# Performance work log

Hardware: AMD Instinct MI355X
Metric: run time of the kernel (lower is better)

The kernel has to match this reference:

```python
import jax, jax.numpy as jnp
import numpy as np

B, S, D, H = 2, 2048, 2048, 16
HD = D // H

def setup_inputs() -> dict:
    key = jax.random.key(0)
    ks = jax.random.split(key, 6)
    x = jax.random.normal(ks[0], (B, S, D), dtype=jnp.float32)
    # causal mask: 1 where attention allowed, 0 where masked
    mask = jnp.tril(jnp.ones((S, S), dtype=jnp.int32))[None, None, :, :]
    scale_w = 0.02
    W_qkv = jax.random.normal(ks[1], (D, 3 * D), dtype=jnp.float32) * scale_w
    b_qkv = jnp.zeros((3 * D,), dtype=jnp.float32)
    W_proj = jax.random.normal(ks[2], (D, D), dtype=jnp.float32) * scale_w
    b_proj = jnp.zeros((D,), dtype=jnp.float32)
    return {"x": x, "W_qkv": W_qkv, "b_qkv": b_qkv, "W_proj": W_proj, "b_proj": b_proj, "mask": mask}

def reference(x, W_qkv, b_qkv, W_proj, b_proj, mask):
    b, s, d = x.shape
    qkv = x @ W_qkv + b_qkv                       # [b,s,3d]
    qkv = qkv.reshape(b, s, 3, H, HD)
    q = jnp.transpose(qkv[:, :, 0], (0, 2, 1, 3))  # [b,h,s,hd]
    k = jnp.transpose(qkv[:, :, 1], (0, 2, 1, 3))
    v = jnp.transpose(qkv[:, :, 2], (0, 2, 1, 3))
    scale = HD ** -0.5
    attn = jnp.einsum('bhqd,bhkd->bhqk', q, k) * scale
    attn = jnp.where(mask == 0, -jnp.inf, attn)
    attn = jax.nn.softmax(attn, axis=-1)
    # dropout is identity in eval mode
    out = jnp.einsum('bhqk,bhkd->bhqd', attn, v)   # [b,h,s,hd]
    out = jnp.transpose(out, (0, 2, 1, 3)).reshape(b, s, d)
    return out @ W_proj + b_proj
```

## Files before the change

### kernel.cpp

```cpp
#include <hip/hip_runtime.h>
#include <hip/hip_bf16.h>
#include <math.h>

#define BATCH 2
#define SEQ   2048
#define DIM   2048
#define NH    16
#define HD    128
#define QKV_N (3 * DIM)
#define TOKENS (BATCH * SEQ)

typedef __attribute__((ext_vector_type(8))) short bf16x8;
typedef __attribute__((ext_vector_type(4))) float f32x4;

typedef __attribute__((address_space(1))) const void* as1cv;
typedef __attribute__((address_space(3))) void* as3v;

__device__ __forceinline__ short f2bf(float x) {
    unsigned u = __float_as_uint(x);
    u += 0x7fffu + ((u >> 16) & 1u);
    return (short)(u >> 16);
}

__device__ __forceinline__ float bf2f(short x) {
    return __uint_as_float(((unsigned)(unsigned short)x) << 16);
}

__device__ __forceinline__ void gload16(const short* g, short* lds) {
    __builtin_amdgcn_global_load_lds((as1cv)g, (as3v)lds, 16, 0, 0);
}

__global__ __launch_bounds__(256)
void f32_to_bf16_kernel(const float* __restrict__ in, short* __restrict__ out) {
    const size_t i = ((size_t)blockIdx.x * 256 + threadIdx.x) * 8;
    const float4 a = *reinterpret_cast<const float4*>(in + i);
    const float4 b = *reinterpret_cast<const float4*>(in + i + 4);
    bf16x8 v;
    v[0] = f2bf(a.x); v[1] = f2bf(a.y); v[2] = f2bf(a.z); v[3] = f2bf(a.w);
    v[4] = f2bf(b.x); v[5] = f2bf(b.y); v[6] = f2bf(b.z); v[7] = f2bf(b.w);
    *reinterpret_cast<bf16x8*>(out + i) = v;
}

__global__ __launch_bounds__(256)
void transpose_f32_to_bf16(const float* __restrict__ W, short* __restrict__ Wt,
                           int K, int N) {
    __shared__ float t[64][65];
    const int tid = threadIdx.x;
    const int n0 = blockIdx.x * 64;
    const int k0 = blockIdx.y * 64;
    const int tc = tid & 63, tr = tid >> 6;
    #pragma unroll
    for (int i = 0; i < 16; ++i)
        t[tr + i * 4][tc] = W[(size_t)(k0 + tr + i * 4) * N + n0 + tc];
    __syncthreads();
    #pragma unroll
    for (int i = 0; i < 16; ++i)
        Wt[(size_t)(n0 + tr + i * 4) * K + k0 + tc] = f2bf(t[tc][tr + i * 4]);
}

template <bool BF16OUT>
__global__ __launch_bounds__(256, 2)
void gemm_mfma_kernel(const short* __restrict__ A, const short* __restrict__ Bt,
                      const float* __restrict__ bias, void* __restrict__ Cv,
                      int M, int N, int K, int nM) {
    __shared__ short A_lds[2][128 * 64];
    __shared__ short B_lds[2][128 * 64];

    const int tid  = threadIdx.x;
    const int lane = tid & 63;
    const int w    = tid >> 6;
    const int lr   = lane & 15;
    const int lhi  = lane >> 4;
    const int wr   = w >> 1;
    const int wc   = w & 1;

    const int nwg  = gridDim.x;
    const int cpx  = nwg >> 3;
    const int orig = blockIdx.x;
    const int wg   = (orig & 7) * cpx + (orig >> 3);
    const int bm   = (wg % nM) * 128;
    const int bn   = (wg / nM) * 128;

    const int srow   = tid >> 3;
    const int schunk = (tid & 7) ^ (srow & 7);
    const short* gA = A  + (size_t)(bm + srow) * K + schunk * 8;
    const short* gB = Bt + (size_t)(bn + srow) * K + schunk * 8;

    const int nt = K >> 6;

    auto STAGE = [&](int t, int buf) {
        const int ko = t * 64;
        short* la = &A_lds[buf][w * 512];
        short* lb = &B_lds[buf][w * 512];
        #pragma unroll
        for (int i = 0; i < 4; ++i)
            gload16(gA + (size_t)(i * 32) * K + ko, la + i * 2048);
        #pragma unroll
        for (int i = 0; i < 4; ++i)
            gload16(gB + (size_t)(i * 32) * K + ko, lb + i * 2048);
    };

    f32x4 acc[4][4] = {};

    STAGE(0, 0);
    STAGE(1, 1);
    asm volatile("s_waitcnt vmcnt(8)" ::: "memory");
    __builtin_amdgcn_s_barrier();

    int cur = 0;
    for (int t = 0; t < nt; ++t, cur ^= 1) {
        bf16x8 af[2][4], bfr[2][4];
        const short* Ab = &A_lds[cur][0];
        const short* Bb = &B_lds[cur][0];
        #pragma unroll
        for (int ks = 0; ks < 2; ++ks) {
            const int cb = ks * 4 + lhi;
            #pragma unroll
            for (int mi = 0; mi < 4; ++mi) {
                const int r = wr * 64 + mi * 16 + lr;
                af[ks][mi] = *reinterpret_cast<const bf16x8*>(
                    &Ab[r * 64 + ((cb ^ (r & 7)) << 3)]);
            }
            #pragma unroll
            for (int ni = 0; ni < 4; ++ni) {
                const int c = wc * 64 + ni * 16 + lr;
                bfr[ks][ni] = *reinterpret_cast<const bf16x8*>(
                    &Bb[c * 64 + ((cb ^ (c & 7)) << 3)]);
            }
        }
        asm volatile("s_waitcnt lgkmcnt(0)" ::: "memory");
        __builtin_amdgcn_sched_barrier(0);
        __builtin_amdgcn_s_barrier();
        __builtin_amdgcn_sched_barrier(0);

        if (t + 2 < nt) STAGE(t + 2, cur);

        __builtin_amdgcn_s_setprio(1);
        #pragma unroll
        for (int ks = 0; ks < 2; ++ks)
            #pragma unroll
            for (int mi = 0; mi < 4; ++mi)
                #pragma unroll
                for (int ni = 0; ni < 4; ++ni)
                    acc[mi][ni] = __builtin_amdgcn_mfma_f32_16x16x32_bf16(
                        af[ks][mi], bfr[ks][ni], acc[mi][ni], 0, 0, 0);
        __builtin_amdgcn_s_setprio(0);
        __builtin_amdgcn_sched_barrier(0);

        if (t + 2 < nt) {
            asm volatile("s_waitcnt vmcnt(8)" ::: "memory");
            __builtin_amdgcn_s_barrier();
        } else if (t + 1 < nt) {
            asm volatile("s_waitcnt vmcnt(0)" ::: "memory");
            __builtin_amdgcn_s_barrier();
        }
    }

    #pragma unroll
    for (int mi = 0; mi < 4; ++mi) {
        #pragma unroll
        for (int j = 0; j < 4; ++j) {
            const int r = bm + wr * 64 + mi * 16 + lhi * 4 + j;
            #pragma unroll
            for (int ni = 0; ni < 4; ++ni) {
                const int c = bn + wc * 64 + ni * 16 + lr;
                const float v = acc[mi][ni][j] + bias[c];
                if (BF16OUT) ((short*)Cv)[(size_t)r * N + c] = f2bf(v);
                else         ((float*)Cv)[(size_t)r * N + c] = v;
            }
        }
    }
}

__device__ __forceinline__ int swz8(int row) {
    return ((row ^ (row >> 2)) & 7) << 3;
}

__global__ __launch_bounds__(256)
void attn_mfma_kernel(const short* __restrict__ qkv, short* __restrict__ out) {
    __shared__ short K_lds[64 * 128];
    __shared__ short V_lds[128 * 64];
    __shared__ short P_lds[4 * 16 * 64];

    const int tid  = threadIdx.x;
    const int lane = tid & 63;
    const int w    = tid >> 6;

    const int z    = blockIdx.x;
    const int qblk = (SEQ / 64 - 1) - (z >> 5);
    const int bh   = z & 31;
    const int h    = bh & 15;
    const int b    = bh >> 4;

    const int q0 = qblk * 64;
    const size_t tokbase = (size_t)b * SEQ * QKV_N;

    const int lr  = lane & 15;
    const int lhi = lane >> 4;
    const float scale = 0.08838834764831845f;

    const int qrow = q0 + w * 16 + lr;
    const short* qrowp = qkv + tokbase + (size_t)qrow * QKV_N + h * HD;
    bf16x8 qfrag[4];
    #pragma unroll
    for (int ks = 0; ks < 4; ++ks) {
        bf16x8 v = *reinterpret_cast<const bf16x8*>(qrowp + ks * 32 + lhi * 8);
        bf16x8 sv;
        #pragma unroll
        for (int e = 0; e < 8; ++e) sv[e] = f2bf(bf2f(v[e]) * scale);
        qfrag[ks] = sv;
    }

    f32x4 o[8] = {};
    float m[4], l[4];
    #pragma unroll
    for (int j = 0; j < 4; ++j) { m[j] = -3.0e38f; l[j] = 0.f; }

    const int wq0 = q0 + w * 16;
    const int ntiles = qblk + 1;

    for (int t = 0; t < ntiles; ++t) {
        {
            const int r  = tid >> 2;
            const int q4 = tid & 3;
            const short* krow = qkv + tokbase + (size_t)(t * 64 + r) * QKV_N
                                + DIM + h * HD + q4 * 32;
            short* kdst = &K_lds[r * 128];
            #pragma unroll
            for (int cc = 0; cc < 4; ++cc) {
                bf16x8 kv8 = *reinterpret_cast<const bf16x8*>(krow + cc * 8);
                *reinterpret_cast<bf16x8*>(kdst + ((q4 * 32 + cc * 8) ^ swz8(r))) = kv8;
            }
        }
        {
            const int p  = tid >> 3;
            const int c  = tid & 7;
            const int kv = p * 2;
            const int kc = kv >> 3;
            const short* vrow = qkv + tokbase + (size_t)(t * 64 + kv) * QKV_N
                                + 2 * DIM + h * HD + c * 16;
            #pragma unroll
            for (int half = 0; half < 2; ++half) {
                const bf16x8 va = *reinterpret_cast<const bf16x8*>(vrow + half * 8);
                const bf16x8 vb = *reinterpret_cast<const bf16x8*>(vrow + QKV_N + half * 8);
                #pragma unroll
                for (int dd = 0; dd < 8; ++dd) {
                    const int d  = c * 16 + half * 8 + dd;
                    const int sw = ((d >> 4) ^ d) & 7;
                    const unsigned pk = ((unsigned)(unsigned short)va[dd]) |
                                        (((unsigned)(unsigned short)vb[dd]) << 16);
                    *reinterpret_cast<unsigned*>(
                        &V_lds[d * 64 + ((kc ^ sw) << 3) + (kv & 7)]) = pk;
                }
            }
        }
        __syncthreads();

        f32x4 s[4] = {};
        #pragma unroll
        for (int ks = 0; ks < 4; ++ks) {
            #pragma unroll
            for (int cg = 0; cg < 4; ++cg) {
                const int row = cg * 16 + lr;
                const bf16x8 kf = *reinterpret_cast<const bf16x8*>(
                    &K_lds[row * 128 + ((ks * 32 + lhi * 8) ^ swz8(row))]);
                s[cg] = __builtin_amdgcn_mfma_f32_16x16x32_bf16(qfrag[ks], kf, s[cg], 0, 0, 0);
            }
        }

        const bool diag = (t == qblk);
        #pragma unroll
        for (int j = 0; j < 4; ++j) {
            if (diag) {
                const int qg = wq0 + lhi * 4 + j;
                #pragma unroll
                for (int cg = 0; cg < 4; ++cg) {
                    const int kvg = t * 64 + cg * 16 + lr;
                    if (kvg > qg) s[cg][j] = -3.0e38f;
                }
            }
            float mx = fmaxf(fmaxf(s[0][j], s[1][j]), fmaxf(s[2][j], s[3][j]));
            #pragma unroll
            for (int off = 1; off < 16; off <<= 1) mx = fmaxf(mx, __shfl_xor(mx, off));
            const float mnew = fmaxf(m[j], mx);
            const float corr = __expf(m[j] - mnew);
            m[j] = mnew;
            float rsum = 0.f;
            #pragma unroll
            for (int cg = 0; cg < 4; ++cg) {
                const float e = __expf(s[cg][j] - mnew);
                s[cg][j] = e;
                rsum += e;
            }
            #pragma unroll
            for (int off = 1; off < 16; off <<= 1) rsum += __shfl_xor(rsum, off);
            l[j] = l[j] * corr + rsum;
            #pragma unroll
            for (int cg = 0; cg < 8; ++cg) o[cg][j] *= corr;
        }

        short* pbase = &P_lds[w * 1024];
        #pragma unroll
        for (int cg = 0; cg < 4; ++cg) {
            #pragma unroll
            for (int j = 0; j < 4; ++j) {
                const int rw = lhi * 4 + j;
                const int c  = cg * 16 + lr;
                pbase[rw * 64 + (c ^ swz8(rw))] = f2bf(s[cg][j]);
            }
        }
        bf16x8 pa[2];
        #pragma unroll
        for (int ks = 0; ks < 2; ++ks)
            pa[ks] = *reinterpret_cast<const bf16x8*>(
                &pbase[lr * 64 + ((ks * 32 + lhi * 8) ^ swz8(lr))]);

        #pragma unroll
        for (int cg = 0; cg < 8; ++cg) {
            const int d  = cg * 16 + lr;
            const int sw = ((d >> 4) ^ d) & 7;
            #pragma unroll
            for (int ks = 0; ks < 2; ++ks) {
                const bf16x8 vf = *reinterpret_cast<const bf16x8*>(
                    &V_lds[d * 64 + (((ks * 4 + lhi) ^ sw) << 3)]);
                o[cg] = __builtin_amdgcn_mfma_f32_16x16x32_bf16(pa[ks], vf, o[cg], 0, 0, 0);
            }
        }
        __syncthreads();
    }

    #pragma unroll
    for (int j = 0; j < 4; ++j) {
        const float inv = 1.f / l[j];
        const int qg = q0 + w * 16 + lhi * 4 + j;
        short* op = out + (size_t)(b * SEQ + qg) * DIM + h * HD;
        #pragma unroll
        for (int cg = 0; cg < 8; ++cg)
            op[cg * 16 + lr] = f2bf(o[cg][j] * inv);
    }
}

extern "C" void kernel_launch(void* const* d_in, const int* in_sizes, int n_in,
                              void* d_out, int out_size, void* d_ws, size_t ws_size,
                              hipStream_t stream) {
    const float* x      = (const float*)d_in[0];
    const float* W_qkv  = (const float*)d_in[1];
    const float* b_qkv  = (const float*)d_in[2];
    const float* W_proj = (const float*)d_in[3];
    const float* b_proj = (const float*)d_in[4];

    float* out = (float*)d_out;

    short* qkv_bf  = (short*)d_ws;
    short* attn_bf = qkv_bf  + (size_t)TOKENS * QKV_N;
    short* x_bf    = attn_bf + (size_t)TOKENS * DIM;
    short* wqkv_t  = x_bf    + (size_t)TOKENS * DIM;
    short* wproj_t = wqkv_t  + (size_t)DIM * QKV_N;

    f32_to_bf16_kernel<<<TOKENS * DIM / (256 * 8), 256, 0, stream>>>(x, x_bf);
    {
        dim3 g(QKV_N / 64, DIM / 64);
        transpose_f32_to_bf16<<<g, 256, 0, stream>>>(W_qkv, wqkv_t, DIM, QKV_N);
    }
    {
        dim3 g(DIM / 64, DIM / 64);
        transpose_f32_to_bf16<<<g, 256, 0, stream>>>(W_proj, wproj_t, DIM, DIM);
    }

    {
        const int nM = TOKENS / 128, nN = QKV_N / 128;
        gemm_mfma_kernel<true><<<nM * nN, 256, 0, stream>>>(
            x_bf, wqkv_t, b_qkv, (void*)qkv_bf, TOKENS, QKV_N, DIM, nM);
    }
    attn_mfma_kernel<<<BATCH * NH * (SEQ / 64), 256, 0, stream>>>(qkv_bf, attn_bf);

    {
        const int nM = TOKENS / 128, nN = DIM / 128;
        gemm_mfma_kernel<false><<<nM * nN, 256, 0, stream>>>(
            attn_bf, wproj_t, b_proj, (void*)out, TOKENS, DIM, DIM, nM);
    }
}
```

Measured before the change: 271.8 us.

## Use 128-row query blocks with 8 waves sharing K/V tiles in attention

```diff
diff --git a/kernel.cpp b/kernel.cpp
--- a/kernel.cpp
+++ b/kernel.cpp
@@ -176,30 +176,31 @@
     return ((row ^ (row >> 2)) & 7) << 3;
 }
 
-__global__ __launch_bounds__(256)
+__global__ __launch_bounds__(512)
 void attn_mfma_kernel(const short* __restrict__ qkv, short* __restrict__ out) {
     __shared__ short K_lds[64 * 128];
     __shared__ short V_lds[128 * 64];
-    __shared__ short P_lds[4 * 16 * 64];
+    __shared__ short P_lds[8 * 16 * 64];
 
     const int tid  = threadIdx.x;
     const int lane = tid & 63;
     const int w    = tid >> 6;
 
     const int z    = blockIdx.x;
-    const int qblk = (SEQ / 64 - 1) - (z >> 5);
+    const int qblk = (z < 256) ? (15 - (z >> 5)) : ((z - 256) >> 5);
     const int bh   = z & 31;
     const int h    = bh & 15;
     const int b    = bh >> 4;
 
-    const int q0 = qblk * 64;
+    const int q0 = qblk * 128;
     const size_t tokbase = (size_t)b * SEQ * QKV_N;
 
     const int lr  = lane & 15;
     const int lhi = lane >> 4;
     const float scale = 0.08838834764831845f;
 
-    const int qrow = q0 + w * 16 + lr;
+    const int wq0  = q0 + w * 16;
+    const int qrow = wq0 + lr;
     const short* qrowp = qkv + tokbase + (size_t)qrow * QKV_N + h * HD;
     bf16x8 qfrag[4];
     #pragma unroll
@@ -216,114 +217,113 @@
     #pragma unroll
     for (int j = 0; j < 4; ++j) { m[j] = -3.0e38f; l[j] = 0.f; }
 
-    const int wq0 = q0 + w * 16;
-    const int ntiles = qblk + 1;
+    const int diag   = wq0 >> 6;
+    const int ntiles = 2 * qblk + 2;
+
+    const int k_rl = tid >> 4;
+    const int k_st = tid & 15;
+    const int v_p  = tid >> 4;
+    const int v_c8 = tid & 15;
 
     for (int t = 0; t < ntiles; ++t) {
         {
-            const int r  = tid >> 2;
-            const int q4 = tid & 3;
-            const short* krow = qkv + tokbase + (size_t)(t * 64 + r) * QKV_N
-                                + DIM + h * HD + q4 * 32;
-            short* kdst = &K_lds[r * 128];
-            #pragma unroll
-            for (int cc = 0; cc < 4; ++cc) {
-                bf16x8 kv8 = *reinterpret_cast<const bf16x8*>(krow + cc * 8);
-                *reinterpret_cast<bf16x8*>(kdst + ((q4 * 32 + cc * 8) ^ swz8(r))) = kv8;
+            const short* kb = qkv + tokbase + (size_t)(t * 64) * QKV_N + DIM + h * HD;
+            #pragma unroll
+            for (int i = 0; i < 2; ++i) {
+                const int row = i * 32 + k_rl;
+                const short* src = kb + (size_t)row * QKV_N + ((k_st << 3) ^ swz8(row));
+                gload16(src, &K_lds[(i * 32 + w * 4) * 128]);
             }
         }
         {
-            const int p  = tid >> 3;
-            const int c  = tid & 7;
-            const int kv = p * 2;
+            const int kv = v_p * 2;
             const int kc = kv >> 3;
             const short* vrow = qkv + tokbase + (size_t)(t * 64 + kv) * QKV_N
-                                + 2 * DIM + h * HD + c * 16;
-            #pragma unroll
-            for (int half = 0; half < 2; ++half) {
-                const bf16x8 va = *reinterpret_cast<const bf16x8*>(vrow + half * 8);
-                const bf16x8 vb = *reinterpret_cast<const bf16x8*>(vrow + QKV_N + half * 8);
-                #pragma unroll
-                for (int dd = 0; dd < 8; ++dd) {
-                    const int d  = c * 16 + half * 8 + dd;
-                    const int sw = ((d >> 4) ^ d) & 7;
-                    const unsigned pk = ((unsigned)(unsigned short)va[dd]) |
-                                        (((unsigned)(unsigned short)vb[dd]) << 16);
-                    *reinterpret_cast<unsigned*>(
-                        &V_lds[d * 64 + ((kc ^ sw) << 3) + (kv & 7)]) = pk;
-                }
+                                + 2 * DIM + h * HD + v_c8 * 8;
+            const bf16x8 va = *reinterpret_cast<const bf16x8*>(vrow);
+            const bf16x8 vb = *reinterpret_cast<const bf16x8*>(vrow + QKV_N);
+            #pragma unroll
+            for (int dd = 0; dd < 8; ++dd) {
+                const int d  = v_c8 * 8 + dd;
+                const int sw = (((d >> 4) & 7) ^ (d & 7));
+                const unsigned pk = ((unsigned)(unsigned short)va[dd]) |
+                                    (((unsigned)(unsigned short)vb[dd]) << 16);
+                *reinterpret_cast<unsigned*>(
+                    &V_lds[d * 64 + ((kc ^ sw) << 3) + (kv & 7)]) = pk;
             }
         }
         __syncthreads();
 
-        f32x4 s[4] = {};
-        #pragma unroll
-        for (int ks = 0; ks < 4; ++ks) {
+        if (t <= diag) {
+            f32x4 s[4] = {};
+            #pragma unroll
+            for (int ks = 0; ks < 4; ++ks) {
+                #pragma unroll
+                for (int cg = 0; cg < 4; ++cg) {
+                    const int row = cg * 16 + lr;
+                    const bf16x8 kf = *reinterpret_cast<const bf16x8*>(
+                        &K_lds[row * 128 + ((ks * 32 + lhi * 8) ^ swz8(row))]);
+                    s[cg] = __builtin_amdgcn_mfma_f32_16x16x32_bf16(qfrag[ks], kf, s[cg], 0, 0, 0);
+                }
+            }
+
+            const bool dmask = (t == diag);
+            #pragma unroll
+            for (int j = 0; j < 4; ++j) {
+                if (dmask) {
+                    const int qg = wq0 + lhi * 4 + j;
+                    #pragma unroll
+                    for (int cg = 0; cg < 4; ++cg) {
+                        const int kvg = t * 64 + cg * 16 + lr;
+                        if (kvg > qg) s[cg][j] = -3.0e38f;
+                    }
+                }
+                float mx = fmaxf(fmaxf(s[0][j], s[1][j]), fmaxf(s[2][j], s[3][j]));
+                #pragma unroll
+                for (int off = 1; off < 16; off <<= 1) mx = fmaxf(mx, __shfl_xor(mx, off));
+                const float mnew = fmaxf(m[j], mx);
+                const float corr = __expf(m[j] - mnew);
+                m[j] = mnew;
+                float rsum = 0.f;
+                #pragma unroll
+                for (int cg = 0; cg < 4; ++cg) {
+                    const float e = __expf(s[cg][j] - mnew);
+                    s[cg][j] = e;
+                    rsum += e;
+                }
+                #pragma unroll
+                for (int off = 1; off < 16; off <<= 1) rsum += __shfl_xor(rsum, off);
+                l[j] = l[j] * corr + rsum;
+                #pragma unroll
+                for (int cg = 0; cg < 8; ++cg) o[cg][j] *= corr;
+            }
+
+            short* pbase = &P_lds[w * 1024];
             #pragma unroll
             for (int cg = 0; cg < 4; ++cg) {
-                const int row = cg * 16 + lr;
-                const bf16x8 kf = *reinterpret_cast<const bf16x8*>(
-                    &K_lds[row * 128 + ((ks * 32 + lhi * 8) ^ swz8(row))]);
-                s[cg] = __builtin_amdgcn_mfma_f32_16x16x32_bf16(qfrag[ks], kf, s[cg], 0, 0, 0);
-            }
-        }
-
-        const bool diag = (t == qblk);
-        #pragma unroll
-        for (int j = 0; j < 4; ++j) {
-            if (diag) {
-                const int qg = wq0 + lhi * 4 + j;
-                #pragma unroll
-                for (int cg = 0; cg < 4; ++cg) {
-                    const int kvg = t * 64 + cg * 16 + lr;
-                    if (kvg > qg) s[cg][j] = -3.0e38f;
-                }
-            }
-            float mx = fmaxf(fmaxf(s[0][j], s[1][j]), fmaxf(s[2][j], s[3][j]));
-            #pragma unroll
-            for (int off = 1; off < 16; off <<= 1) mx = fmaxf(mx, __shfl_xor(mx, off));
-            const float mnew = fmaxf(m[j], mx);
-            const float corr = __expf(m[j] - mnew);
-            m[j] = mnew;
-            float rsum = 0.f;
-            #pragma unroll
-            for (int cg = 0; cg < 4; ++cg) {
-                const float e = __expf(s[cg][j] - mnew);
-                s[cg][j] = e;
-                rsum += e;
-            }
-            #pragma unroll
-            for (int off = 1; off < 16; off <<= 1) rsum += __shfl_xor(rsum, off);
-            l[j] = l[j] * corr + rsum;
-            #pragma unroll
-            for (int cg = 0; cg < 8; ++cg) o[cg][j] *= corr;
-        }
-
-        short* pbase = &P_lds[w * 1024];
-        #pragma unroll
-        for (int cg = 0; cg < 4; ++cg) {
-            #pragma unroll
-            for (int j = 0; j < 4; ++j) {
-                const int rw = lhi * 4 + j;
-                const int c  = cg * 16 + lr;
-                pbase[rw * 64 + (c ^ swz8(rw))] = f2bf(s[cg][j]);
-            }
-        }
-        bf16x8 pa[2];
-        #pragma unroll
-        for (int ks = 0; ks < 2; ++ks)
-            pa[ks] = *reinterpret_cast<const bf16x8*>(
-                &pbase[lr * 64 + ((ks * 32 + lhi * 8) ^ swz8(lr))]);
-
-        #pragma unroll
-        for (int cg = 0; cg < 8; ++cg) {
-            const int d  = cg * 16 + lr;
-            const int sw = ((d >> 4) ^ d) & 7;
-            #pragma unroll
-            for (int ks = 0; ks < 2; ++ks) {
-                const bf16x8 vf = *reinterpret_cast<const bf16x8*>(
-                    &V_lds[d * 64 + (((ks * 4 + lhi) ^ sw) << 3)]);
-                o[cg] = __builtin_amdgcn_mfma_f32_16x16x32_bf16(pa[ks], vf, o[cg], 0, 0, 0);
+                #pragma unroll
+                for (int j = 0; j < 4; ++j) {
+                    const int rw = lhi * 4 + j;
+                    const int c  = cg * 16 + lr;
+                    pbase[rw * 64 + (c ^ swz8(rw))] = f2bf(s[cg][j]);
+                }
+            }
+            bf16x8 pa[2];
+            #pragma unroll
+            for (int ks = 0; ks < 2; ++ks)
+                pa[ks] = *reinterpret_cast<const bf16x8*>(
+                    &pbase[lr * 64 + ((ks * 32 + lhi * 8) ^ swz8(lr))]);
+
+            #pragma unroll
+            for (int cg = 0; cg < 8; ++cg) {
+                const int d  = cg * 16 + lr;
+                const int sw = (((d >> 4) & 7) ^ (d & 7));
+                #pragma unroll
+                for (int ks = 0; ks < 2; ++ks) {
+                    const bf16x8 vf = *reinterpret_cast<const bf16x8*>(
+                        &V_lds[d * 64 + (((ks * 4 + lhi) ^ sw) << 3)]);
+                    o[cg] = __builtin_amdgcn_mfma_f32_16x16x32_bf16(pa[ks], vf, o[cg], 0, 0, 0);
+                }
             }
         }
         __syncthreads();
@@ -332,7 +332,7 @@
     #pragma unroll
     for (int j = 0; j < 4; ++j) {
         const float inv = 1.f / l[j];
-        const int qg = q0 + w * 16 + lhi * 4 + j;
+        const int qg = wq0 + lhi * 4 + j;
         short* op = out + (size_t)(b * SEQ + qg) * DIM + h * HD;
         #pragma unroll
         for (int cg = 0; cg < 8; ++cg)
@@ -372,7 +372,7 @@
         gemm_mfma_kernel<true><<<nM * nN, 256, 0, stream>>>(
             x_bf, wqkv_t, b_qkv, (void*)qkv_bf, TOKENS, QKV_N, DIM, nM);
     }
-    attn_mfma_kernel<<<BATCH * NH * (SEQ / 64), 256, 0, stream>>>(qkv_bf, attn_bf);
+    attn_mfma_kernel<<<BATCH * NH * (SEQ / 128), 512, 0, stream>>>(qkv_bf, attn_bf);
 
     {
         const int nM = TOKENS / 128, nN = DIM / 128;
```

After: 311.5 us. 14.6% more time.
